# Performance work log

Hardware: AMD Instinct MI355X
Metric: run time of the kernel (lower is better)

Reference implementation:

```python
import jax, jax.numpy as jnp
import numpy as np

B, S, H, E, NF, NM = 4096, 512, 5, 4, 1, 64  # batch, seq, hidden, embed_dim, numeric feats, num_mote_ids
D = NF + E  # lstm input size = 5


def setup_inputs() -> dict:
    key = jax.random.key(0)
    k = jax.random.split(key, 7)
    s = 1.0 / np.sqrt(H)  # PyTorch LSTM init scale
    return {
        "x_num": jax.random.normal(k[0], (B, S, NF), jnp.float32),
        "x_cat": jax.random.randint(k[1], (B, S, 1), 0, NM, jnp.int32),
        "embed": jax.random.normal(k[2], (NM, E), jnp.float32),
        "W_ih": jax.random.uniform(k[3], (4 * H, D), jnp.float32, -s, s),
        "W_hh": jax.random.uniform(k[4], (4 * H, H), jnp.float32, -s, s),
        "b_ih": jax.random.uniform(k[5], (4 * H,), jnp.float32, -s, s),
        "b_hh": jax.random.uniform(k[6], (4 * H,), jnp.float32, -s, s),
    }


def reference(x_num, x_cat, embed, W_ih, W_hh, b_ih, b_hh):
    # embedding lookup + concat -> [B, S, D]
    emb = embed[x_cat[:, :, 0]]
    x = jnp.concatenate([x_num, emb], axis=2)
    # precompute input-to-gate projections once: [B, S, 4H]
    xg = jnp.einsum('bsd,gd->bsg', x, W_ih) + b_ih + b_hh

    def step(carry, xt):  # xt: [B, 4H]
        h, c = carry
        g = xt + h @ W_hh.T
        i, f, gg, o = jnp.split(g, 4, axis=-1)  # PyTorch gate order: i, f, g, o
        i = jax.nn.sigmoid(i)
        f = jax.nn.sigmoid(f)
        gg = jnp.tanh(gg)
        o = jax.nn.sigmoid(o)
        c = f * c + i * gg
        h = o * jnp.tanh(c)
        return (h, c), h

    h0 = jnp.zeros((B, H), x.dtype)
    c0 = jnp.zeros((B, H), x.dtype)
    (hT, cT), outs = jax.lax.scan(step, (h0, c0), jnp.swapaxes(xg, 0, 1))
    out = jnp.swapaxes(outs, 0, 1)  # [B, S, H]
    return out, hT[None], cT[None]  # hidden/cell: [num_layers=1, B, H]
```

## Files before the change

### kernel.cpp

```cpp
#include <hip/hip_runtime.h>

#define NBATCH 4096
#define SEQ 512
#define HID 5
#define NEMB 64

__device__ __forceinline__ float fexp2(float x){ return __builtin_amdgcn_exp2f(x); }
__device__ __forceinline__ float frcp(float x){ return __builtin_amdgcn_rcpf(x); }

#define DPPQ(v, j) __int_as_float(__builtin_amdgcn_update_dpp(0, __float_as_int(v), ((j) * 0x55), 0xF, 0xF, true))
#define DPPM(old, src, CTRL, BANKS) __int_as_float(__builtin_amdgcn_update_dpp(__float_as_int(old), __float_as_int(src), (CTRL), 0xF, (BANKS), false))
#define ROW_SHL4 0x104
#define ROW_SHR4 0x114

__global__ __launch_bounds__(64) void lstm_enc_kernel(
    const float* __restrict__ x_num, const int* __restrict__ x_cat,
    const float* __restrict__ embed, const float* __restrict__ W_ih,
    const float* __restrict__ W_hh, const float* __restrict__ b_ih,
    const float* __restrict__ b_hh, float* __restrict__ out)
{
    __shared__ float4 s_emb[NEMB];
    int tid = threadIdx.x;
    s_emb[tid] = ((const float4*)embed)[tid];
    __syncthreads();

    int gid = blockIdx.x * 64 + tid;
    int b   = gid >> 3;
    int sub = tid & 7;
    int k   = (sub < HID) ? sub : (HID - 1);
    bool active = (sub < HID);

    const float L2E = 1.4426950408889634f;
    const float sc[4] = {-L2E, -L2E, -2.0f * L2E, -L2E};

    float wi[4][5], wh[4][5], bb[4];
#pragma unroll
    for (int q = 0; q < 4; ++q) {
        float s = sc[q];
        int g = q * HID + k;
#pragma unroll
        for (int d = 0; d < 5; ++d) {
            wi[q][d] = W_ih[g * 5 + d] * s;
            wh[q][d] = W_hh[g * HID + d] * s;
        }
        bb[q] = (b_ih[g] + b_hh[g]) * s;
    }

    const float4* xp = (const float4*)(x_num + (size_t)b * SEQ);
    const int4*   cp = (const int4*)(x_cat + (size_t)b * SEQ);
    float* outp = out + (size_t)b * SEQ * HID + k;

    float h = 0.0f, c = 0.0f;

    float4 xf = xp[0];
    int4   cf = cp[0];
    float4 ec_[4];
    ec_[0] = s_emb[cf.x]; ec_[1] = s_emb[cf.y];
    ec_[2] = s_emb[cf.z]; ec_[3] = s_emb[cf.w];

    for (int t0 = 0; t0 < SEQ; t0 += 4) {
        int nidx = (t0 + 4 < SEQ) ? ((t0 >> 2) + 1) : 0;
        float4 xf_n = xp[nidx];
        int4   cf_n = cp[nidx];

        float xn_a[4] = {xf.x, xf.y, xf.z, xf.w};

        float xa[4][4];
#pragma unroll
        for (int u = 0; u < 4; ++u) {
            float4 e = ec_[u];
#pragma unroll
            for (int q = 0; q < 4; ++q) {
                float a = fmaf(xn_a[u], wi[q][0], bb[q]);
                a = fmaf(e.x, wi[q][1], a);
                a = fmaf(e.y, wi[q][2], a);
                a = fmaf(e.z, wi[q][3], a);
                a = fmaf(e.w, wi[q][4], a);
                xa[u][q] = a;
            }
        }

#pragma unroll
        for (int u = 0; u < 4; ++u) {
            float q0 = DPPQ(h, 0);
            float q1 = DPPQ(h, 1);
            float q2 = DPPQ(h, 2);
            float q3 = DPPQ(h, 3);
            float hb0 = DPPM(q0, q0, ROW_SHR4, 0xA);
            float hb1 = DPPM(q1, q1, ROW_SHR4, 0xA);
            float hb2 = DPPM(q2, q2, ROW_SHR4, 0xA);
            float hb3 = DPPM(q3, q3, ROW_SHR4, 0xA);
            float hb4 = DPPM(h,  h,  ROW_SHL4, 0x5);

            float a0 = xa[u][0], a1 = xa[u][1], a2 = xa[u][2], a3 = xa[u][3];
            a0 = fmaf(hb0, wh[0][0], a0);
            a1 = fmaf(hb0, wh[1][0], a1);
            a2 = fmaf(hb0, wh[2][0], a2);
            a3 = fmaf(hb0, wh[3][0], a3);
            a0 = fmaf(hb1, wh[0][1], a0);
            a1 = fmaf(hb1, wh[1][1], a1);
            a2 = fmaf(hb1, wh[2][1], a2);
            a3 = fmaf(hb1, wh[3][1], a3);
            a0 = fmaf(hb2, wh[0][2], a0);
            a1 = fmaf(hb2, wh[1][2], a1);
            a2 = fmaf(hb2, wh[2][2], a2);
            a3 = fmaf(hb2, wh[3][2], a3);
            a0 = fmaf(hb3, wh[0][3], a0);
            a1 = fmaf(hb3, wh[1][3], a1);
            a2 = fmaf(hb3, wh[2][3], a2);
            a3 = fmaf(hb3, wh[3][3], a3);
            a0 = fmaf(hb4, wh[0][4], a0);
            a1 = fmaf(hb4, wh[1][4], a1);
            a2 = fmaf(hb4, wh[2][4], a2);
            a3 = fmaf(hb4, wh[3][4], a3);

            float iv = frcp(1.0f + fexp2(a0));
            float fv = frcp(1.0f + fexp2(a1));
            float gv = fmaf(frcp(1.0f + fexp2(a2)), 2.0f, -1.0f);
            float ov = frcp(1.0f + fexp2(a3));

            c = fmaf(fv, c, iv * gv);
            float tc = fmaf(frcp(1.0f + fexp2(c * (-2.0f * L2E))), 2.0f, -1.0f);
            h = ov * tc;

            if (active) outp[(t0 + u) * HID] = h;
        }

        ec_[0] = s_emb[cf_n.x]; ec_[1] = s_emb[cf_n.y];
        ec_[2] = s_emb[cf_n.z]; ec_[3] = s_emb[cf_n.w];
        xf = xf_n;
    }

    if (active) {
        size_t base = (size_t)NBATCH * SEQ * HID;
        out[base + (size_t)b * HID + k] = h;
        out[base + (size_t)NBATCH * HID + (size_t)b * HID + k] = c;
    }
}

extern "C" void kernel_launch(void* const* d_in, const int* in_sizes, int n_in,
                              void* d_out, int out_size, void* d_ws, size_t ws_size,
                              hipStream_t stream) {
    const float* x_num = (const float*)d_in[0];
    const int*   x_cat = (const int*)d_in[1];
    const float* embed = (const float*)d_in[2];
    const float* W_ih  = (const float*)d_in[3];
    const float* W_hh  = (const float*)d_in[4];
    const float* b_ih  = (const float*)d_in[5];
    const float* b_hh  = (const float*)d_in[6];
    float* out = (float*)d_out;

    dim3 grid(NBATCH * 8 / 64);
    dim3 block(64);
    hipLaunchKernelGGL(lstm_enc_kernel, grid, block, 0, stream,
                       x_num, x_cat, embed, W_ih, W_hh, b_ih, b_hh, out);
}
```

Before: 109.0 us.

## Split LSTM gates across lanes: one lane per (hidden unit, gate)

Remaps the work so each batch element uses 32 lanes (20 active), with one lane per hidden unit and gate pair, instead of 8 lanes holding all four gates per hidden unit. Each lane now does a single 5-term recurrent dot product and one sigmoid. Gate values are gathered with quad DPP broadcasts and h is redistributed with ds_swizzle. This shortens each lane's serial chain per timestep, but the grid grows fourfold (2048 blocks), more lanes sit idle, and ds_swizzle goes through the LDS crossbar with higher latency than DPP.

New measurement: 89.44 us. 1.22x faster.

```diff
diff --git a/kernel.cpp b/kernel.cpp
--- a/kernel.cpp
+++ b/kernel.cpp
@@ -8,10 +8,8 @@
 __device__ __forceinline__ float fexp2(float x){ return __builtin_amdgcn_exp2f(x); }
 __device__ __forceinline__ float frcp(float x){ return __builtin_amdgcn_rcpf(x); }
 
+#define SWZ(v, k) __int_as_float(__builtin_amdgcn_ds_swizzle(__float_as_int(v), ((4*(k)) << 5)))
 #define DPPQ(v, j) __int_as_float(__builtin_amdgcn_update_dpp(0, __float_as_int(v), ((j) * 0x55), 0xF, 0xF, true))
-#define DPPM(old, src, CTRL, BANKS) __int_as_float(__builtin_amdgcn_update_dpp(__float_as_int(old), __float_as_int(src), (CTRL), 0xF, (BANKS), false))
-#define ROW_SHL4 0x104
-#define ROW_SHR4 0x114
 
 __global__ __launch_bounds__(64) void lstm_enc_kernel(
     const float* __restrict__ x_num, const int* __restrict__ x_cat,
@@ -24,33 +22,33 @@
     s_emb[tid] = ((const float4*)embed)[tid];
     __syncthreads();
 
-    int gid = blockIdx.x * 64 + tid;
-    int b   = gid >> 3;
-    int sub = tid & 7;
-    int k   = (sub < HID) ? sub : (HID - 1);
-    bool active = (sub < HID);
+    int half = tid >> 5;
+    int l    = tid & 31;
+    int b    = blockIdx.x * 2 + half;
+    int k    = ((l >> 2) < HID) ? (l >> 2) : (HID - 1);
+    int g    = l & 3;
+    bool st  = (l < 20) && (g == 0);
 
     const float L2E = 1.4426950408889634f;
-    const float sc[4] = {-L2E, -L2E, -2.0f * L2E, -L2E};
+    float s_  = (g == 2) ? (-2.0f * L2E) : (-L2E);
+    float fm  = (g == 2) ? 2.0f : 1.0f;
+    float fb  = (g == 2) ? -1.0f : 0.0f;
 
-    float wi[4][5], wh[4][5], bb[4];
+    int row = g * HID + k;
+    float wi_[5], wh_[5];
 #pragma unroll
-    for (int q = 0; q < 4; ++q) {
-        float s = sc[q];
-        int g = q * HID + k;
-#pragma unroll
-        for (int d = 0; d < 5; ++d) {
-            wi[q][d] = W_ih[g * 5 + d] * s;
-            wh[q][d] = W_hh[g * HID + d] * s;
-        }
-        bb[q] = (b_ih[g] + b_hh[g]) * s;
+    for (int d = 0; d < 5; ++d) {
+        wi_[d] = W_ih[row * 5 + d] * s_;
+        wh_[d] = W_hh[row * 5 + d] * s_;
     }
+    float bias = (b_ih[row] + b_hh[row]) * s_;
 
     const float4* xp = (const float4*)(x_num + (size_t)b * SEQ);
     const int4*   cp = (const int4*)(x_cat + (size_t)b * SEQ);
     float* outp = out + (size_t)b * SEQ * HID + k;
 
-    float h = 0.0f, c = 0.0f;
+    float h = 0.f, c = 0.f;
+    float hb0 = 0.f, hb1 = 0.f, hb2 = 0.f, hb3 = 0.f, hb4 = 0.f;
 
     float4 xf = xp[0];
     int4   cf = cp[0];
@@ -65,65 +63,46 @@
 
         float xn_a[4] = {xf.x, xf.y, xf.z, xf.w};
 
-        float xa[4][4];
+        float xa[4];
 #pragma unroll
         for (int u = 0; u < 4; ++u) {
             float4 e = ec_[u];
-#pragma unroll
-            for (int q = 0; q < 4; ++q) {
-                float a = fmaf(xn_a[u], wi[q][0], bb[q]);
-                a = fmaf(e.x, wi[q][1], a);
-                a = fmaf(e.y, wi[q][2], a);
-                a = fmaf(e.z, wi[q][3], a);
-                a = fmaf(e.w, wi[q][4], a);
-                xa[u][q] = a;
-            }
+            float a = fmaf(xn_a[u], wi_[0], bias);
+            a = fmaf(e.x, wi_[1], a);
+            a = fmaf(e.y, wi_[2], a);
+            a = fmaf(e.z, wi_[3], a);
+            a = fmaf(e.w, wi_[4], a);
+            xa[u] = a;
         }
 
 #pragma unroll
         for (int u = 0; u < 4; ++u) {
-            float q0 = DPPQ(h, 0);
-            float q1 = DPPQ(h, 1);
-            float q2 = DPPQ(h, 2);
-            float q3 = DPPQ(h, 3);
-            float hb0 = DPPM(q0, q0, ROW_SHR4, 0xA);
-            float hb1 = DPPM(q1, q1, ROW_SHR4, 0xA);
-            float hb2 = DPPM(q2, q2, ROW_SHR4, 0xA);
-            float hb3 = DPPM(q3, q3, ROW_SHR4, 0xA);
-            float hb4 = DPPM(h,  h,  ROW_SHL4, 0x5);
+            float a = xa[u];
+            a = fmaf(hb0, wh_[0], a);
+            a = fmaf(hb1, wh_[1], a);
+            a = fmaf(hb2, wh_[2], a);
+            a = fmaf(hb3, wh_[3], a);
+            a = fmaf(hb4, wh_[4], a);
 
-            float a0 = xa[u][0], a1 = xa[u][1], a2 = xa[u][2], a3 = xa[u][3];
-            a0 = fmaf(hb0, wh[0][0], a0);
-            a1 = fmaf(hb0, wh[1][0], a1);
-            a2 = fmaf(hb0, wh[2][0], a2);
-            a3 = fmaf(hb0, wh[3][0], a3);
-            a0 = fmaf(hb1, wh[0][1], a0);
-            a1 = fmaf(hb1, wh[1][1], a1);
-            a2 = fmaf(hb1, wh[2][1], a2);
-            a3 = fmaf(hb1, wh[3][1], a3);
-            a0 = fmaf(hb2, wh[0][2], a0);
-            a1 = fmaf(hb2, wh[1][2], a1);
-            a2 = fmaf(hb2, wh[2][2], a2);
-            a3 = fmaf(hb2, wh[3][2], a3);
-            a0 = fmaf(hb3, wh[0][3], a0);
-            a1 = fmaf(hb3, wh[1][3], a1);
-            a2 = fmaf(hb3, wh[2][3], a2);
-            a3 = fmaf(hb3, wh[3][3], a3);
-            a0 = fmaf(hb4, wh[0][4], a0);
-            a1 = fmaf(hb4, wh[1][4], a1);
-            a2 = fmaf(hb4, wh[2][4], a2);
-            a3 = fmaf(hb4, wh[3][4], a3);
+            float r = frcp(1.0f + fexp2(a));
+            float v = fmaf(r, fm, fb);
 
-            float iv = frcp(1.0f + fexp2(a0));
-            float fv = frcp(1.0f + fexp2(a1));
-            float gv = fmaf(frcp(1.0f + fexp2(a2)), 2.0f, -1.0f);
-            float ov = frcp(1.0f + fexp2(a3));
+            float ai = DPPQ(v, 0);
+            float af = DPPQ(v, 1);
+            float ag = DPPQ(v, 2);
+            float ao = DPPQ(v, 3);
 
-            c = fmaf(fv, c, iv * gv);
+            c = fmaf(af, c, ai * ag);
             float tc = fmaf(frcp(1.0f + fexp2(c * (-2.0f * L2E))), 2.0f, -1.0f);
-            h = ov * tc;
+            h = ao * tc;
 
-            if (active) outp[(t0 + u) * HID] = h;
+            hb0 = SWZ(h, 0);
+            hb1 = SWZ(h, 1);
+            hb2 = SWZ(h, 2);
+            hb3 = SWZ(h, 3);
+            hb4 = SWZ(h, 4);
+
+            if (st) outp[(t0 + u) * HID] = h;
         }
 
         ec_[0] = s_emb[cf_n.x]; ec_[1] = s_emb[cf_n.y];
@@ -131,7 +110,7 @@
         xf = xf_n;
     }
 
-    if (active) {
+    if (st) {
         size_t base = (size_t)NBATCH * SEQ * HID;
         out[base + (size_t)b * HID + k] = h;
         out[base + (size_t)NBATCH * HID + (size_t)b * HID + k] = c;
@@ -150,7 +129,7 @@
     const float* b_hh  = (const float*)d_in[6];
     float* out = (float*)d_out;
 
-    dim3 grid(NBATCH * 8 / 64);
+    dim3 grid(NBATCH / 2);
     dim3 block(64);
     hipLaunchKernelGGL(lstm_enc_kernel, grid, block, 0, stream,
                        x_num, x_cat, embed, W_ih, W_hh, b_ih, b_hh, out);
```
